# Performance work log

Measured on AMD Instinct MI355X. Metric: run time of the kernel, lower is better.

Reference implementation:

```python
import jax, jax.numpy as jnp
import numpy as np

B, T, C = 4, 2048, 1024
WIN = 16


def setup_inputs() -> dict:
    key = jax.random.key(0)
    ks = jax.random.split(key, 5)
    s = 1.0 / np.sqrt(C)
    return {
        "x": jax.random.normal(ks[0], (B, T, C), dtype=jnp.float32),
        "Wq": jax.random.normal(ks[1], (C, C), dtype=jnp.float32) * s,
        "bq": jnp.zeros((C,), jnp.float32),
        "Wk": jax.random.normal(ks[2], (C, C), dtype=jnp.float32) * s,
        "bk": jnp.zeros((C,), jnp.float32),
        "Wv": jax.random.normal(ks[3], (C, C), dtype=jnp.float32) * s,
        "bv": jnp.zeros((C,), jnp.float32),
        "Wo": jax.random.normal(ks[4], (C, C), dtype=jnp.float32) * s,
        "bo": jnp.zeros((C,), jnp.float32),
        "window": WIN,
    }


def reference(x, Wq, bq, Wk, bk, Wv, bv, Wo, bo, window):
    Bn, Tn, Cn = x.shape
    half = window // 2
    W = 2 * half + 1  # keys per query (window [t-half, t+half])
    q = x @ Wq.T + bq
    k = x @ Wk.T + bk
    v = x @ Wv.T + bv
    offs = jnp.arange(-half, half + 1)              # [W]
    tpos = jnp.arange(Tn)                            # [T]
    idx = tpos[:, None] + offs[None, :]              # [T, W]
    valid = (idx >= 0) & (idx < Tn)                  # [T, W]
    idx_c = jnp.clip(idx, 0, Tn - 1)
    k_win = k[:, idx_c, :]                           # [B, T, W, C]
    v_win = v[:, idx_c, :]                           # [B, T, W, C]
    scale = 1.0 / jnp.sqrt(jnp.asarray(Cn, x.dtype))
    scores = jnp.einsum('btc,btwc->btw', q, k_win) * scale
    scores = jnp.where(valid[None, :, :], scores, jnp.finfo(x.dtype).min)
    attn = jax.nn.softmax(scores, axis=-1)           # [B, T, W]
    ctx = jnp.einsum('btw,btwc->btc', attn, v_win)   # [B, T, C]
    return ctx @ Wo.T + bo
```

## Files before the change

### kernel.cpp

```cpp
#include <hip/hip_runtime.h>
#include <cstdint>
#include <cstddef>

#define B_ 4
#define T_ 2048
#define C_ 1024
#define M_ (B_ * T_)
#define HALF_ 8
#define W_ 17
#define QKV_STRIDE 3072

typedef unsigned short u16;
typedef _Float16 half8 __attribute__((ext_vector_type(8)));
typedef float f32x4 __attribute__((ext_vector_type(4)));

__device__ __forceinline__ void gload_lds16(const u16* g, u16* l) {
#if __has_builtin(__builtin_amdgcn_global_load_lds)
    __builtin_amdgcn_global_load_lds(
        (const __attribute__((address_space(1))) void*)g,
        (__attribute__((address_space(3))) void*)l, 16, 0, 0);
#else
    *(uint4*)(l + (threadIdx.x & 63) * 8) = *(const uint4*)g;
#endif
}

__global__ void cvt_f32_f16(const float* __restrict__ in, u16* __restrict__ out, int n4) {
    int i = blockIdx.x * blockDim.x + threadIdx.x;
    if (i >= n4) return;
    float4 v = ((const float4*)in)[i];
    ushort4 o;
    _Float16 a = (_Float16)v.x; o.x = __builtin_bit_cast(unsigned short, a);
    _Float16 b = (_Float16)v.y; o.y = __builtin_bit_cast(unsigned short, b);
    _Float16 c = (_Float16)v.z; o.z = __builtin_bit_cast(unsigned short, c);
    _Float16 d = (_Float16)v.w; o.w = __builtin_bit_cast(unsigned short, d);
    ((ushort4*)out)[i] = o;
}

__global__ void cvt_wqkv(const float* __restrict__ Wq, const float* __restrict__ Wk,
                         const float* __restrict__ Wv, u16* __restrict__ out) {
    int i = blockIdx.x * 256 + threadIdx.x;
    int sel = blockIdx.x >> 10;
    const float* src = (sel == 0) ? Wq : (sel == 1) ? Wk : Wv;
    int j = i - (sel << 18);
    float4 v = ((const float4*)src)[j];
    ushort4 o;
    _Float16 a = (_Float16)v.x; o.x = __builtin_bit_cast(unsigned short, a);
    _Float16 b = (_Float16)v.y; o.y = __builtin_bit_cast(unsigned short, b);
    _Float16 c = (_Float16)v.z; o.z = __builtin_bit_cast(unsigned short, c);
    _Float16 d = (_Float16)v.w; o.w = __builtin_bit_cast(unsigned short, d);
    ((ushort4*)out)[i] = o;
}

__global__ void build_bias(const float* __restrict__ bq, const float* __restrict__ bk,
                           const float* __restrict__ bv, float* __restrict__ bcat) {
    int i = blockIdx.x * 256 + threadIdx.x;
    const float* src = (i < 1024) ? bq : (i < 2048) ? bk : bv;
    bcat[i] = src[i & 1023];
}

template <int OUT_F16>
__global__ __launch_bounds__(256) void gemm_nt_lds(
    const u16* __restrict__ A, const u16* __restrict__ Bw,
    const float* __restrict__ bias, void* __restrict__ Cout,
    int Ndim, int Kdim)
{
    __shared__ __align__(16) u16 As[128 * 32];
    __shared__ __align__(16) u16 Bs[128 * 32];

    const int tid  = threadIdx.x;
    const int lane = tid & 63;
    const int wave = tid >> 6;
    const int m0 = blockIdx.y * 128;
    const int n0 = blockIdx.x * 128;
    const int wm = (wave >> 1) * 64;
    const int wn = (wave & 1) * 64;

    const int srow = wave * 32 + (lane >> 2);
    const int scol = (lane & 3) * 8;
    const u16* Ap = A  + (size_t)(m0 + srow) * Kdim + scol;
    const u16* Bp = Bw + (size_t)(n0 + srow) * Kdim + scol;
    const size_t skip16 = (size_t)16 * Kdim;
    u16* AsW = As + wave * 1024;
    u16* BsW = Bs + wave * 1024;

    f32x4 zero = {0.f, 0.f, 0.f, 0.f};
    f32x4 acc[4][4];
#pragma unroll
    for (int i = 0; i < 4; ++i)
#pragma unroll
        for (int j = 0; j < 4; ++j) acc[i][j] = zero;

    const int fr = lane & 15;
    const int fk = (lane >> 4) * 8;

    for (int k0 = 0; k0 < Kdim; k0 += 32) {
        __syncthreads();
        gload_lds16(Ap + k0,          AsW);
        gload_lds16(Ap + k0 + skip16, AsW + 512);
        gload_lds16(Bp + k0,          BsW);
        gload_lds16(Bp + k0 + skip16, BsW + 512);
        __syncthreads();

        half8 af[4], bf[4];
#pragma unroll
        for (int i = 0; i < 4; ++i)
            af[i] = *(const half8*)&As[(wm + i * 16 + fr) * 32 + fk];
#pragma unroll
        for (int j = 0; j < 4; ++j)
            bf[j] = *(const half8*)&Bs[(wn + j * 16 + fr) * 32 + fk];
#pragma unroll
        for (int i = 0; i < 4; ++i)
#pragma unroll
            for (int j = 0; j < 4; ++j)
                acc[i][j] = __builtin_amdgcn_mfma_f32_16x16x32_f16(af[i], bf[j], acc[i][j], 0, 0, 0);
    }

#pragma unroll
    for (int i = 0; i < 4; ++i) {
        const int row0 = m0 + wm + i * 16 + (lane >> 4) * 4;
#pragma unroll
        for (int j = 0; j < 4; ++j) {
            const int col = n0 + wn + j * 16 + (lane & 15);
            const float bv = bias[col];
#pragma unroll
            for (int r = 0; r < 4; ++r) {
                float val = acc[i][j][r] + bv;
                if (OUT_F16) {
                    _Float16 h = (_Float16)val;
                    ((u16*)Cout)[(size_t)(row0 + r) * Ndim + col] = __builtin_bit_cast(unsigned short, h);
                } else {
                    ((float*)Cout)[(size_t)(row0 + r) * Ndim + col] = val;
                }
            }
        }
    }
}

__global__ __launch_bounds__(256) void attn_local(
    const u16* __restrict__ qkv, u16* __restrict__ ctx)
{
    const int wid  = blockIdx.x * 4 + (threadIdx.x >> 6);
    const int lane = threadIdx.x & 63;
    const int b = wid >> 11;
    const int t = wid & (T_ - 1);
    const size_t qrow = (size_t)(b * T_ + t) * QKV_STRIDE;
    const int c0 = lane * 8;

    half8 q0 = *(const half8*)(qkv + qrow + c0);
    half8 q1 = *(const half8*)(qkv + qrow + 512 + c0);

    float s[W_];
#pragma unroll
    for (int o = 0; o < W_; ++o) {
        int j = t - HALF_ + o;
        if (j >= 0 && j < T_) {
            const size_t kb = (size_t)(b * T_ + j) * QKV_STRIDE + 1024;
            half8 k0v = *(const half8*)(qkv + kb + c0);
            half8 k1v = *(const half8*)(qkv + kb + 512 + c0);
            float d = 0.f;
#pragma unroll
            for (int e = 0; e < 8; ++e)
                d += (float)q0[e] * (float)k0v[e] + (float)q1[e] * (float)k1v[e];
#pragma unroll
            for (int off = 32; off > 0; off >>= 1)
                d += __shfl_xor(d, off);
            s[o] = d * 0.03125f;
        } else {
            s[o] = -3.0e38f;
        }
    }

    float mx = s[0];
#pragma unroll
    for (int o = 1; o < W_; ++o) mx = fmaxf(mx, s[o]);
    float w[W_];
    float den = 0.f;
#pragma unroll
    for (int o = 0; o < W_; ++o) { w[o] = __expf(s[o] - mx); den += w[o]; }
    const float inv = 1.f / den;

    float acc0[8], acc1[8];
#pragma unroll
    for (int e = 0; e < 8; ++e) { acc0[e] = 0.f; acc1[e] = 0.f; }
#pragma unroll
    for (int o = 0; o < W_; ++o) {
        int j = t - HALF_ + o;
        if (j < 0 || j >= T_) continue;
        const float wt = w[o] * inv;
        const size_t vb_ = (size_t)(b * T_ + j) * QKV_STRIDE + 2048;
        half8 v0 = *(const half8*)(qkv + vb_ + c0);
        half8 v1 = *(const half8*)(qkv + vb_ + 512 + c0);
#pragma unroll
        for (int e = 0; e < 8; ++e) {
            acc0[e] += wt * (float)v0[e];
            acc1[e] += wt * (float)v1[e];
        }
    }

    const size_t crow = (size_t)(b * T_ + t) * C_;
    half8 o0, o1;
#pragma unroll
    for (int e = 0; e < 8; ++e) { o0[e] = (_Float16)acc0[e]; o1[e] = (_Float16)acc1[e]; }
    *(half8*)(ctx + crow + c0) = o0;
    *(half8*)(ctx + crow + 512 + c0) = o1;
}

extern "C" void kernel_launch(void* const* d_in, const int* in_sizes, int n_in,
                              void* d_out, int out_size, void* d_ws, size_t ws_size,
                              hipStream_t stream) {
    const float* x  = (const float*)d_in[0];
    const float* Wq = (const float*)d_in[1];
    const float* bq = (const float*)d_in[2];
    const float* Wk = (const float*)d_in[3];
    const float* bk = (const float*)d_in[4];
    const float* Wv = (const float*)d_in[5];
    const float* bv = (const float*)d_in[6];
    const float* Wo = (const float*)d_in[7];
    const float* bo = (const float*)d_in[8];
    float* out = (float*)d_out;

    u16* xh   = (u16*)d_ws;
    u16* wcat = xh   + (size_t)M_ * C_;
    u16* woh  = wcat + (size_t)3 * C_ * C_;
    u16* qkvh = woh  + (size_t)C_ * C_;
    u16* ctxh = qkvh + (size_t)M_ * QKV_STRIDE;
    float* bcat = (float*)(ctxh + (size_t)M_ * C_);

    const int nx4 = M_ * C_ / 4;
    cvt_f32_f16<<<nx4 / 256, 256, 0, stream>>>(x, xh, nx4);
    cvt_wqkv<<<3 * 1024, 256, 0, stream>>>(Wq, Wk, Wv, wcat);
    cvt_f32_f16<<<1024, 256, 0, stream>>>(Wo, woh, C_ * C_ / 4);
    build_bias<<<12, 256, 0, stream>>>(bq, bk, bv, bcat);

    dim3 gqkv(QKV_STRIDE / 128, M_ / 128);
    gemm_nt_lds<1><<<gqkv, 256, 0, stream>>>(xh, wcat, bcat, qkvh, QKV_STRIDE, C_);

    attn_local<<<M_ / 4, 256, 0, stream>>>(qkvh, ctxh);

    dim3 go(C_ / 128, M_ / 128);
    gemm_nt_lds<0><<<go, 256, 0, stream>>>(ctxh, woh, bo, out, C_, C_);
}
```

Baseline: 258.0 us.

## Fuse conversion kernels, swizzle GEMM LDS layout, use fdot2 in local attention

Merges the four fp32-to-fp16 conversion and bias-concat launches into one prologue kernel to cut launch overhead. Applies an XOR swizzle to the LDS k-chunk placement in the MFMA GEMM to reduce bank conflicts on fragment reads. In the attention kernel, replaces the scalar fp16 dot products with fdot2 intrinsics and makes the window loop branchless by clamping indices and masking scores. It also recomputes exp instead of storing weights, which frees registers at the cost of extra transcendental work and redundant loads at sequence edges.

```diff
diff --git a/kernel.cpp b/kernel.cpp
--- a/kernel.cpp
+++ b/kernel.cpp
@@ -12,6 +12,7 @@
 
 typedef unsigned short u16;
 typedef _Float16 half8 __attribute__((ext_vector_type(8)));
+typedef _Float16 half2_t __attribute__((ext_vector_type(2)));
 typedef float f32x4 __attribute__((ext_vector_type(4)));
 
 __device__ __forceinline__ void gload_lds16(const u16* g, u16* l) {
@@ -24,38 +25,51 @@
 #endif
 }
 
-__global__ void cvt_f32_f16(const float* __restrict__ in, u16* __restrict__ out, int n4) {
-    int i = blockIdx.x * blockDim.x + threadIdx.x;
-    if (i >= n4) return;
-    float4 v = ((const float4*)in)[i];
-    ushort4 o;
-    _Float16 a = (_Float16)v.x; o.x = __builtin_bit_cast(unsigned short, a);
-    _Float16 b = (_Float16)v.y; o.y = __builtin_bit_cast(unsigned short, b);
-    _Float16 c = (_Float16)v.z; o.z = __builtin_bit_cast(unsigned short, c);
-    _Float16 d = (_Float16)v.w; o.w = __builtin_bit_cast(unsigned short, d);
-    ((ushort4*)out)[i] = o;
-}
-
-__global__ void cvt_wqkv(const float* __restrict__ Wq, const float* __restrict__ Wk,
-                         const float* __restrict__ Wv, u16* __restrict__ out) {
-    int i = blockIdx.x * 256 + threadIdx.x;
-    int sel = blockIdx.x >> 10;
-    const float* src = (sel == 0) ? Wq : (sel == 1) ? Wk : Wv;
-    int j = i - (sel << 18);
+__device__ __forceinline__ float dot16(half8 a, half8 b, float acc) {
+#if __has_builtin(__builtin_amdgcn_fdot2)
+    const half2_t* pa = (const half2_t*)&a;
+    const half2_t* pb = (const half2_t*)&b;
+#pragma unroll
+    for (int e = 0; e < 4; ++e) acc = __builtin_amdgcn_fdot2(pa[e], pb[e], acc, false);
+#else
+#pragma unroll
+    for (int e = 0; e < 8; ++e) acc += (float)a[e] * (float)b[e];
+#endif
+    return acc;
+}
+
+__global__ void prologue(const float* __restrict__ x,
+                         const float* __restrict__ Wq, const float* __restrict__ Wk,
+                         const float* __restrict__ Wv, const float* __restrict__ Wo,
+                         const float* __restrict__ bq, const float* __restrict__ bk,
+                         const float* __restrict__ bv,
+                         u16* __restrict__ xh, u16* __restrict__ wcat,
+                         u16* __restrict__ woh, float* __restrict__ bcat) {
+    const int blk = blockIdx.x;
+    if (blk >= 12288) {
+        int i = (blk - 12288) * 256 + threadIdx.x;
+        const float* src = (i < 1024) ? bq : (i < 2048) ? bk : bv;
+        bcat[i] = src[i & 1023];
+        return;
+    }
+    const float* src;
+    u16* dst;
+    int j;
+    if (blk < 8192)       { src = x;  dst = xh;   j = blk * 256 + threadIdx.x; }
+    else if (blk < 11264) {
+        int bb = blk - 8192;
+        int sel = bb >> 10;
+        src = (sel == 0) ? Wq : (sel == 1) ? Wk : Wv;
+        dst = wcat + ((size_t)sel << 20);
+        j = (bb - (sel << 10)) * 256 + threadIdx.x;
+    } else                { src = Wo; dst = woh;  j = (blk - 11264) * 256 + threadIdx.x; }
     float4 v = ((const float4*)src)[j];
     ushort4 o;
     _Float16 a = (_Float16)v.x; o.x = __builtin_bit_cast(unsigned short, a);
     _Float16 b = (_Float16)v.y; o.y = __builtin_bit_cast(unsigned short, b);
     _Float16 c = (_Float16)v.z; o.z = __builtin_bit_cast(unsigned short, c);
     _Float16 d = (_Float16)v.w; o.w = __builtin_bit_cast(unsigned short, d);
-    ((ushort4*)out)[i] = o;
-}
-
-__global__ void build_bias(const float* __restrict__ bq, const float* __restrict__ bk,
-                           const float* __restrict__ bv, float* __restrict__ bcat) {
-    int i = blockIdx.x * 256 + threadIdx.x;
-    const float* src = (i < 1024) ? bq : (i < 2048) ? bk : bv;
-    bcat[i] = src[i & 1023];
+    ((ushort4*)dst)[j] = o;
 }
 
 template <int OUT_F16>
@@ -76,9 +90,9 @@
     const int wn = (wave & 1) * 64;
 
     const int srow = wave * 32 + (lane >> 2);
-    const int scol = (lane & 3) * 8;
-    const u16* Ap = A  + (size_t)(m0 + srow) * Kdim + scol;
-    const u16* Bp = Bw + (size_t)(n0 + srow) * Kdim + scol;
+    const int kc = ((lane & 3) ^ ((lane >> 3) & 3)) * 8;
+    const u16* Ap = A  + (size_t)(m0 + srow) * Kdim + kc;
+    const u16* Bp = Bw + (size_t)(n0 + srow) * Kdim + kc;
     const size_t skip16 = (size_t)16 * Kdim;
     u16* AsW = As + wave * 1024;
     u16* BsW = Bs + wave * 1024;
@@ -91,7 +105,7 @@
         for (int j = 0; j < 4; ++j) acc[i][j] = zero;
 
     const int fr = lane & 15;
-    const int fk = (lane >> 4) * 8;
+    const int fk = (((lane >> 4) ^ ((lane >> 1) & 3)) & 3) * 8;
 
     for (int k0 = 0; k0 < Kdim; k0 += 32) {
         __syncthreads();
@@ -143,7 +157,8 @@
     const int lane = threadIdx.x & 63;
     const int b = wid >> 11;
     const int t = wid & (T_ - 1);
-    const size_t qrow = (size_t)(b * T_ + t) * QKV_STRIDE;
+    const int base = b * T_;
+    const size_t qrow = (size_t)(base + t) * QKV_STRIDE;
     const int c0 = lane * 8;
 
     half8 q0 = *(const half8*)(qkv + qrow + c0);
@@ -153,30 +168,23 @@
 #pragma unroll
     for (int o = 0; o < W_; ++o) {
         int j = t - HALF_ + o;
-        if (j >= 0 && j < T_) {
-            const size_t kb = (size_t)(b * T_ + j) * QKV_STRIDE + 1024;
-            half8 k0v = *(const half8*)(qkv + kb + c0);
-            half8 k1v = *(const half8*)(qkv + kb + 512 + c0);
-            float d = 0.f;
-#pragma unroll
-            for (int e = 0; e < 8; ++e)
-                d += (float)q0[e] * (float)k0v[e] + (float)q1[e] * (float)k1v[e];
-#pragma unroll
-            for (int off = 32; off > 0; off >>= 1)
-                d += __shfl_xor(d, off);
-            s[o] = d * 0.03125f;
-        } else {
-            s[o] = -3.0e38f;
-        }
+        int jc = min(max(j, 0), T_ - 1);
+        const size_t kb = (size_t)(base + jc) * QKV_STRIDE + 1024;
+        half8 k0v = *(const half8*)(qkv + kb + c0);
+        half8 k1v = *(const half8*)(qkv + kb + 512 + c0);
+        float d = dot16(q1, k1v, dot16(q0, k0v, 0.f));
+#pragma unroll
+        for (int off = 32; off > 0; off >>= 1)
+            d += __shfl_xor(d, off);
+        s[o] = (j == jc) ? d * 0.03125f : -3.0e38f;
     }
 
     float mx = s[0];
 #pragma unroll
     for (int o = 1; o < W_; ++o) mx = fmaxf(mx, s[o]);
-    float w[W_];
     float den = 0.f;
 #pragma unroll
-    for (int o = 0; o < W_; ++o) { w[o] = __expf(s[o] - mx); den += w[o]; }
+    for (int o = 0; o < W_; ++o) den += __expf(s[o] - mx);
     const float inv = 1.f / den;
 
     float acc0[8], acc1[8];
@@ -185,9 +193,9 @@
 #pragma unroll
     for (int o = 0; o < W_; ++o) {
         int j = t - HALF_ + o;
-        if (j < 0 || j >= T_) continue;
-        const float wt = w[o] * inv;
-        const size_t vb_ = (size_t)(b * T_ + j) * QKV_STRIDE + 2048;
+        int jc = min(max(j, 0), T_ - 1);
+        const float wt = __expf(s[o] - mx) * inv;
+        const size_t vb_ = (size_t)(base + jc) * QKV_STRIDE + 2048;
         half8 v0 = *(const half8*)(qkv + vb_ + c0);
         half8 v1 = *(const half8*)(qkv + vb_ + 512 + c0);
 #pragma unroll
@@ -197,7 +205,7 @@
         }
     }
 
-    const size_t crow = (size_t)(b * T_ + t) * C_;
+    const size_t crow = (size_t)(base + t) * C_;
     half8 o0, o1;
 #pragma unroll
     for (int e = 0; e < 8; ++e) { o0[e] = (_Float16)acc0[e]; o1[e] = (_Float16)acc1[e]; }
@@ -226,11 +234,8 @@
     u16* ctxh = qkvh + (size_t)M_ * QKV_STRIDE;
     float* bcat = (float*)(ctxh + (size_t)M_ * C_);
 
-    const int nx4 = M_ * C_ / 4;
-    cvt_f32_f16<<<nx4 / 256, 256, 0, stream>>>(x, xh, nx4);
-    cvt_wqkv<<<3 * 1024, 256, 0, stream>>>(Wq, Wk, Wv, wcat);
-    cvt_f32_f16<<<1024, 256, 0, stream>>>(Wo, woh, C_ * C_ / 4);
-    build_bias<<<12, 256, 0, stream>>>(bq, bk, bv, bcat);
+    prologue<<<12300, 256, 0, stream>>>(x, Wq, Wk, Wv, Wo, bq, bk, bv,
+                                        xh, wcat, woh, bcat);
 
     dim3 gqkv(QKV_STRIDE / 128, M_ / 128);
     gemm_nt_lds<1><<<gqkv, 256, 0, stream>>>(xh, wcat, bcat, qkvh, QKV_STRIDE, C_);
```

After: 247.1 us. 4.2% less time.
